# Kernel tuning notes

Hardware: AMD Instinct MI355X
Metric: run time of the kernel (lower is better)

The kernel has to match this reference:

```python
import jax, jax.numpy as jnp
import numpy as np

N_NODES = 50000
N_EDGES = 1250000
VOCAB = 50000
EMBED = 64
HIDDEN = 64
NUM_REL = 3
N_CLASSES = 2
N_GRAPHS = 512


def setup_inputs() -> dict:
    key = jax.random.key(0)
    ks = jax.random.split(key, 12)
    x = jax.random.randint(ks[0], (N_NODES,), 0, VOCAB, dtype=jnp.int32)
    edge_index = jax.random.randint(ks[1], (2, N_EDGES), 0, N_NODES, dtype=jnp.int32)
    edge_type = jax.random.randint(ks[2], (N_EDGES,), 0, NUM_REL, dtype=jnp.int32)
    batch = jnp.sort(jax.random.randint(ks[3], (N_NODES,), 0, N_GRAPHS, dtype=jnp.int32))
    s = 0.05
    emb = jax.random.normal(ks[4], (VOCAB, EMBED), jnp.float32) * s
    w1_rel = jax.random.normal(ks[5], (NUM_REL, EMBED, HIDDEN), jnp.float32) * s
    w1_root = jax.random.normal(ks[6], (EMBED, HIDDEN), jnp.float32) * s
    b1 = jnp.zeros((HIDDEN,), jnp.float32)
    w2_rel = jax.random.normal(ks[7], (NUM_REL, HIDDEN, HIDDEN), jnp.float32) * s
    w2_root = jax.random.normal(ks[8], (HIDDEN, HIDDEN), jnp.float32) * s
    b2 = jnp.zeros((HIDDEN,), jnp.float32)
    lin_w = jax.random.normal(ks[9], (HIDDEN, N_CLASSES), jnp.float32) * s
    lin_b = jnp.zeros((N_CLASSES,), jnp.float32)
    return {"x": x, "edge_index": edge_index, "edge_type": edge_type, "batch": batch,
            "emb": emb, "w1_rel": w1_rel, "w1_root": w1_root, "b1": b1,
            "w2_rel": w2_rel, "w2_root": w2_root, "b2": b2,
            "lin_w": lin_w, "lin_b": lin_b}


def rgcn_conv(h, src, dst, edge_type, w_rel, w_root, bias):
    # PyG RGCNConv: out = h @ W_root + bias + sum_r mean-aggregated (h_src @ W_r)
    out = h @ w_root + bias
    h_src = h[src]  # [E, F] gather
    for r in range(NUM_REL):
        mask = (edge_type == r).astype(h.dtype)  # [E]
        m = (h_src @ w_rel[r]) * mask[:, None]   # [E, H]
        s = jax.ops.segment_sum(m, dst, num_segments=N_NODES)
        cnt = jax.ops.segment_sum(mask, dst, num_segments=N_NODES)
        out = out + s / jnp.maximum(cnt, 1.0)[:, None]
    return out


def reference(x, edge_index, edge_type, batch, emb, w1_rel, w1_root, b1,
              w2_rel, w2_root, b2, lin_w, lin_b):
    src, dst = edge_index[0], edge_index[1]
    emb_eff = emb.at[0].set(0.0)  # padding_idx=0
    h = emb_eff[x]  # [N, EMBED]
    h = jax.nn.relu(rgcn_conv(h, src, dst, edge_type, w1_rel, w1_root, b1))
    h = jax.nn.relu(rgcn_conv(h, src, dst, edge_type, w2_rel, w2_root, b2))
    # global mean pool over graphs
    sums = jax.ops.segment_sum(h, batch, num_segments=N_GRAPHS)
    cnt = jax.ops.segment_sum(jnp.ones((h.shape[0],), h.dtype), batch, num_segments=N_GRAPHS)
    pooled = sums / jnp.maximum(cnt, 1.0)[:, None]  # [G, HIDDEN]
    return pooled @ lin_w + lin_b  # [G, N_CLASSES]
```

## Files before the change

### kernel.cpp

```cpp
#include <hip/hip_runtime.h>

#define CHUNK 2048

__global__ __launch_bounds__(256) void embed_count_kernel(
    const int* __restrict__ x, const float* __restrict__ emb, float* __restrict__ h0,
    const int* __restrict__ ei, int* __restrict__ pcount,
    int n_nodes, int n_edges, int n_bkt, int n_chk, int embed_blocks)
{
    __shared__ int cnt[512];
    int t = threadIdx.x;
    if ((int)blockIdx.x < embed_blocks) {
        int tt = blockIdx.x * 256 + t;
        if (tt < n_nodes * 16) {
            int n = tt >> 4, q = tt & 15;
            int xv = x[n];
            float4 v = {0.f, 0.f, 0.f, 0.f};
            if (xv != 0) v = *(const float4*)(emb + (size_t)xv * 64 + q * 4);
            *(float4*)(h0 + (size_t)n * 64 + q * 4) = v;
        }
        return;
    }
    int jb = blockIdx.x - embed_blocks;
    for (int b = t; b < 512; b += 256) cnt[b] = 0;
    __syncthreads();
    int base = jb * CHUNK;
#pragma unroll
    for (int i = 0; i < CHUNK / 256; ++i) {
        int e = base + i * 256 + t;
        if (e < n_edges) atomicAdd(&cnt[ei[n_edges + e] >> 7], 1);
    }
    __syncthreads();
    for (int b = t; b < n_bkt; b += 256) pcount[b * n_chk + jb] = cnt[b];
}

__global__ __launch_bounds__(256) void colscan_kernel(
    const int* __restrict__ pcount, int* __restrict__ pre,
    int* __restrict__ totals, int* __restrict__ rowstartR,
    const int* __restrict__ batch, const float* __restrict__ linb,
    float* __restrict__ inv_cnt, float* __restrict__ outg,
    int n_chk, int n_bkt, int n_edges, int n_nodes, int n_graphs)
{
    __shared__ int ps[256];
    int b = blockIdx.x, t = threadIdx.x;
    if (b >= n_bkt) {
        int g = (b - n_bkt) * 256 + t;
        if (g < n_graphs) {
            int lo = 0, hi = n_nodes;
            while (lo < hi) { int mid = (lo + hi) >> 1; if (batch[mid] < g) lo = mid + 1; else hi = mid; }
            int s = lo;
            lo = 0; hi = n_nodes;
            while (lo < hi) { int mid = (lo + hi) >> 1; if (batch[mid] < g + 1) lo = mid + 1; else hi = mid; }
            inv_cnt[g] = 1.f / (float)max(lo - s, 1);
            outg[2 * g + 0] = linb[0];
            outg[2 * g + 1] = linb[1];
        }
        return;
    }
    if (b == 0 && t == 0) rowstartR[4 * n_nodes] = n_edges;
    int v[4], s = 0;
#pragma unroll
    for (int i = 0; i < 4; ++i) {
        int jj = t * 4 + i;
        v[i] = (jj < n_chk) ? pcount[b * n_chk + jj] : 0;
        s += v[i];
    }
    ps[t] = s;
    __syncthreads();
    for (int o = 1; o < 256; o <<= 1) {
        int u = (t >= o) ? ps[t - o] : 0;
        __syncthreads();
        ps[t] += u;
        __syncthreads();
    }
    int run = (t > 0) ? ps[t - 1] : 0;
#pragma unroll
    for (int i = 0; i < 4; ++i) {
        int jj = t * 4 + i;
        if (jj < n_chk) pre[jj * n_bkt + b] = run;
        run += v[i];
    }
    if (t == 255) totals[b] = run;
}

__global__ __launch_bounds__(256) void scatter_kernel(
    const int* __restrict__ ei, const int* __restrict__ et,
    const int* __restrict__ pre, const int* __restrict__ totals,
    int* __restrict__ esort, int* __restrict__ bucket_start,
    int n_edges, int n_bkt)
{
    __shared__ int bs[512], fill2[512], ps[256];
    int t = threadIdx.x, j = blockIdx.x;
    int a0 = (2 * t < n_bkt) ? totals[2 * t] : 0;
    int a1 = (2 * t + 1 < n_bkt) ? totals[2 * t + 1] : 0;
    ps[t] = a0 + a1;
    __syncthreads();
    for (int o = 1; o < 256; o <<= 1) {
        int u = (t >= o) ? ps[t - o] : 0;
        __syncthreads();
        ps[t] += u;
        __syncthreads();
    }
    int basex = (t > 0) ? ps[t - 1] : 0;
    bs[2 * t] = basex;
    bs[2 * t + 1] = basex + a0;
    fill2[t] = 0; fill2[t + 256] = 0;
    __syncthreads();
    if (j == 0) {
        for (int b = t; b < n_bkt; b += 256) bucket_start[b] = bs[b];
        if (t == 0) bucket_start[n_bkt] = n_edges;
    }
    for (int b = t; b < n_bkt; b += 256) bs[b] += pre[j * n_bkt + b];
    __syncthreads();
    int base = j * CHUNK;
#pragma unroll
    for (int i = 0; i < CHUNK / 256; ++i) {
        int e = base + i * 256 + t;
        if (e < n_edges) {
            int s = ei[e], d = ei[n_edges + e], r = et[e];
            int b = d >> 7;
            int pos = bs[b] + atomicAdd(&fill2[b], 1);
            esort[pos] = s | (r << 16) | ((d & 127) << 18);
        }
    }
}

__global__ __launch_bounds__(256) void bucket_sort_kernel(
    const int* __restrict__ bucket_start, const int* __restrict__ esort_in,
    int* __restrict__ esort_out, int* __restrict__ rowstartR, int n_nodes)
{
    __shared__ int cnt[512], off[512], fill[512], ps[256];
    int t = threadIdx.x, b = blockIdx.x;
    int s = bucket_start[b], e = bucket_start[b + 1];
    cnt[t] = 0; cnt[t + 256] = 0; fill[t] = 0; fill[t + 256] = 0;
    __syncthreads();
    for (int i = s + t; i < e; i += 256)
        atomicAdd(&cnt[(esort_in[i] >> 16) & 0x1FF], 1);
    __syncthreads();
    int a0 = cnt[2 * t], a1 = cnt[2 * t + 1];
    ps[t] = a0 + a1;
    __syncthreads();
    for (int o = 1; o < 256; o <<= 1) {
        int v = (t >= o) ? ps[t - o] : 0;
        __syncthreads();
        ps[t] += v;
        __syncthreads();
    }
    int basex = (t > 0) ? ps[t - 1] : 0;
    off[2 * t] = basex;
    off[2 * t + 1] = basex + a0;
    __syncthreads();
    int d0 = b * 128 + (2 * t >> 2);
    if (d0 < n_nodes) rowstartR[b * 512 + 2 * t] = s + off[2 * t];
    int d1 = b * 128 + ((2 * t + 1) >> 2);
    if (d1 < n_nodes) rowstartR[b * 512 + 2 * t + 1] = s + off[2 * t + 1];
    __syncthreads();
    for (int i = s + t; i < e; i += 256) {
        int p = esort_in[i];
        int bin = (p >> 16) & 0x1FF;
        int pos = s + off[bin] + atomicAdd(&fill[bin], 1);
        esort_out[pos] = p;
    }
}

__global__ __launch_bounds__(256) void agg_kernel(
    const float* __restrict__ hin, const int* __restrict__ rowstartR,
    const int* __restrict__ esort, float* __restrict__ means, int n_nodes)
{
    int wid = (blockIdx.x * 256 + threadIdx.x) >> 6;
    int lane = threadIdx.x & 63;
    if (wid >= n_nodes) return;
    int q = lane >> 4;
    int c = lane & 15;
    int4 rs = *(const int4*)(rowstartR + wid * 4);
    int s = rs.x, e = rs.w;

    float4 a0 = {0.f,0.f,0.f,0.f}, a1 = {0.f,0.f,0.f,0.f}, a2 = {0.f,0.f,0.f,0.f};

    int i = s + 4 * q;
    for (; i + 4 <= e; i += 16) {
        int p0 = esort[i], p1 = esort[i + 1], p2 = esort[i + 2], p3 = esort[i + 3];
        float4 v0 = *(const float4*)(hin + (size_t)(p0 & 0xFFFF) * 64 + c * 4);
        float4 v1 = *(const float4*)(hin + (size_t)(p1 & 0xFFFF) * 64 + c * 4);
        float4 v2 = *(const float4*)(hin + (size_t)(p2 & 0xFFFF) * 64 + c * 4);
        float4 v3 = *(const float4*)(hin + (size_t)(p3 & 0xFFFF) * 64 + c * 4);
#pragma unroll
        for (int m = 0; m < 4; ++m) {
            int p = m == 0 ? p0 : m == 1 ? p1 : m == 2 ? p2 : p3;
            float4 v = m == 0 ? v0 : m == 1 ? v1 : m == 2 ? v2 : v3;
            int r = (p >> 16) & 3;
            float m0 = (r == 0) ? 1.f : 0.f;
            float m1 = (r == 1) ? 1.f : 0.f;
            float m2 = (r == 2) ? 1.f : 0.f;
            a0.x = fmaf(m0, v.x, a0.x); a0.y = fmaf(m0, v.y, a0.y);
            a0.z = fmaf(m0, v.z, a0.z); a0.w = fmaf(m0, v.w, a0.w);
            a1.x = fmaf(m1, v.x, a1.x); a1.y = fmaf(m1, v.y, a1.y);
            a1.z = fmaf(m1, v.z, a1.z); a1.w = fmaf(m1, v.w, a1.w);
            a2.x = fmaf(m2, v.x, a2.x); a2.y = fmaf(m2, v.y, a2.y);
            a2.z = fmaf(m2, v.z, a2.z); a2.w = fmaf(m2, v.w, a2.w);
        }
    }
#pragma unroll
    for (int m = 0; m < 3; ++m) {
        int ii = i + m;
        if (ii < e) {
            int p = esort[ii];
            float4 v = *(const float4*)(hin + (size_t)(p & 0xFFFF) * 64 + c * 4);
            int r = (p >> 16) & 3;
            float m0 = (r == 0) ? 1.f : 0.f;
            float m1 = (r == 1) ? 1.f : 0.f;
            float m2 = (r == 2) ? 1.f : 0.f;
            a0.x = fmaf(m0, v.x, a0.x); a0.y = fmaf(m0, v.y, a0.y);
            a0.z = fmaf(m0, v.z, a0.z); a0.w = fmaf(m0, v.w, a0.w);
            a1.x = fmaf(m1, v.x, a1.x); a1.y = fmaf(m1, v.y, a1.y);
            a1.z = fmaf(m1, v.z, a1.z); a1.w = fmaf(m1, v.w, a1.w);
            a2.x = fmaf(m2, v.x, a2.x); a2.y = fmaf(m2, v.y, a2.y);
            a2.z = fmaf(m2, v.z, a2.z); a2.w = fmaf(m2, v.w, a2.w);
        }
    }
#pragma unroll
    for (int off = 16; off < 64; off <<= 1) {
        a0.x += __shfl_xor(a0.x, off); a0.y += __shfl_xor(a0.y, off);
        a0.z += __shfl_xor(a0.z, off); a0.w += __shfl_xor(a0.w, off);
        a1.x += __shfl_xor(a1.x, off); a1.y += __shfl_xor(a1.y, off);
        a1.z += __shfl_xor(a1.z, off); a1.w += __shfl_xor(a1.w, off);
        a2.x += __shfl_xor(a2.x, off); a2.y += __shfl_xor(a2.y, off);
        a2.z += __shfl_xor(a2.z, off); a2.w += __shfl_xor(a2.w, off);
    }
    if (q < 3) {
        int cnt = (q == 0) ? (rs.y - rs.x) : (q == 1) ? (rs.z - rs.y) : (rs.w - rs.z);
        float4 a = (q == 0) ? a0 : (q == 1) ? a1 : a2;
        float inv = 1.f / (float)max(cnt, 1);
        float4 m = {a.x * inv, a.y * inv, a.z * inv, a.w * inv};
        *(float4*)(means + (size_t)wid * 192 + q * 64 + c * 4) = m;
    }
}

__device__ __forceinline__ void stage16(const float* gsrc, float* ldst)
{
    __builtin_amdgcn_global_load_lds(
        (const __attribute__((address_space(1))) unsigned int*)gsrc,
        (__attribute__((address_space(3))) unsigned int*)ldst,
        16, 0, 0);
}

__global__ __launch_bounds__(128, 4) void transform_kernel(
    const float* __restrict__ hin, const float* __restrict__ means,
    const float* __restrict__ wroot, const float* __restrict__ wrel,
    const float* __restrict__ bias, float* __restrict__ hout,
    const int* __restrict__ batch, const float* __restrict__ linw,
    const float* __restrict__ inv_cnt, float* __restrict__ outg,
    int n_nodes, int do_pool)
{
    __shared__ float wsh[2][2048];
    __shared__ float gacc[64][2];
    int t = threadIdx.x;
    int gt = blockIdx.x * 128 + t;
    int g = gt >> 4, q = gt & 15;
    int n0 = g * 4;
    bool active = (n0 < n_nodes);

#pragma unroll
    for (int i = 0; i < 4; ++i)
        stage16(wroot + i * 512 + t * 4, wsh[0] + i * 512 + t * 4);

    float4 acc[4];
    {
        float4 b = {0.f, 0.f, 0.f, 0.f};
        if (active) b = *(const float4*)(bias + q * 4);
#pragma unroll
        for (int i = 0; i < 4; ++i) acc[i] = b;
    }

    const float* hv = hin + (size_t)n0 * 64;
    const float* mv = means + (size_t)n0 * 192;

    for (int ss = 0; ss < 8; ++ss) {
        __syncthreads();
        if (ss < 7) {
            const float* wsrc = (ss + 1 < 2) ? (wroot + (size_t)(ss + 1) * 2048)
                                             : (wrel + (size_t)(ss - 1) * 2048);
            float* d = wsh[(ss + 1) & 1];
#pragma unroll
            for (int i = 0; i < 4; ++i)
                stage16(wsrc + i * 512 + t * 4, d + i * 512 + t * 4);
        }
        int p  = ss >> 1;
        int kb = (ss & 1) * 32;
        const float* vb = ((p == 0) ? hv : (mv + (p - 1) * 64)) + kb;
        int vst = (p == 0) ? 64 : 192;
        const float* wbuf = wsh[ss & 1];
        if (active) {
#pragma unroll
            for (int k4 = 0; k4 < 8; ++k4) {
                float4 v[4];
#pragma unroll
                for (int i = 0; i < 4; ++i)
                    v[i] = *(const float4*)(vb + i * vst + k4 * 4);
#pragma unroll
                for (int kk = 0; kk < 4; ++kk) {
                    float4 w = *(const float4*)(wbuf + (k4 * 4 + kk) * 64 + q * 4);
#pragma unroll
                    for (int i = 0; i < 4; ++i) {
                        float sv = kk == 0 ? v[i].x : kk == 1 ? v[i].y : kk == 2 ? v[i].z : v[i].w;
                        acc[i].x = fmaf(sv, w.x, acc[i].x);
                        acc[i].y = fmaf(sv, w.y, acc[i].y);
                        acc[i].z = fmaf(sv, w.z, acc[i].z);
                        acc[i].w = fmaf(sv, w.w, acc[i].w);
                    }
                }
            }
        }
    }
    if (!do_pool) {
        if (active) {
            float* o = hout + (size_t)n0 * 64 + q * 4;
#pragma unroll
            for (int i = 0; i < 4; ++i) {
                float4 r = {fmaxf(acc[i].x, 0.f), fmaxf(acc[i].y, 0.f),
                            fmaxf(acc[i].z, 0.f), fmaxf(acc[i].w, 0.f)};
                *(float4*)(o + i * 64) = r;
            }
        }
    } else {
        if (t < 64) { gacc[t][0] = 0.f; gacc[t][1] = 0.f; }
        __syncthreads();
        int nbase = blockIdx.x * 32;
        int gmin = batch[min(nbase, n_nodes - 1)];
        if (active) {
            float4 lwA = *(const float4*)(linw + q * 8);
            float4 lwB = *(const float4*)(linw + q * 8 + 4);
            float d0[4], d1[4];
#pragma unroll
            for (int i = 0; i < 4; ++i) {
                float4 r = {fmaxf(acc[i].x, 0.f), fmaxf(acc[i].y, 0.f),
                            fmaxf(acc[i].z, 0.f), fmaxf(acc[i].w, 0.f)};
                d0[i] = r.x * lwA.x + r.y * lwA.z + r.z * lwB.x + r.w * lwB.z;
                d1[i] = r.x * lwA.y + r.y * lwA.w + r.z * lwB.y + r.w * lwB.w;
            }
#pragma unroll
            for (int off = 1; off < 16; off <<= 1) {
#pragma unroll
                for (int i = 0; i < 4; ++i) {
                    d0[i] += __shfl_xor(d0[i], off);
                    d1[i] += __shfl_xor(d1[i], off);
                }
            }
            if (q == 0) {
#pragma unroll
                for (int i = 0; i < 4; ++i) {
                    int n = n0 + i;
                    if (n < n_nodes) {
                        int gg = batch[n];
                        float ic = inv_cnt[gg];
                        int idx = gg - gmin;
                        if (idx < 64) {
                            atomicAdd(&gacc[idx][0], d0[i] * ic);
                            atomicAdd(&gacc[idx][1], d1[i] * ic);
                        } else {
                            atomicAdd(&outg[2 * gg + 0], d0[i] * ic);
                            atomicAdd(&outg[2 * gg + 1], d1[i] * ic);
                        }
                    }
                }
            }
        }
        __syncthreads();
        if (t < 64) {
            float v0 = gacc[t][0], v1 = gacc[t][1];
            if (v0 != 0.f || v1 != 0.f) {
                atomicAdd(&outg[2 * (gmin + t) + 0], v0);
                atomicAdd(&outg[2 * (gmin + t) + 1], v1);
            }
        }
    }
}

extern "C" void kernel_launch(void* const* d_in, const int* in_sizes, int n_in,
                              void* d_out, int out_size, void* d_ws, size_t ws_size,
                              hipStream_t stream)
{
    const int*   x      = (const int*)d_in[0];
    const int*   ei     = (const int*)d_in[1];
    const int*   et     = (const int*)d_in[2];
    const int*   batch  = (const int*)d_in[3];
    const float* emb    = (const float*)d_in[4];
    const float* w1rel  = (const float*)d_in[5];
    const float* w1root = (const float*)d_in[6];
    const float* b1     = (const float*)d_in[7];
    const float* w2rel  = (const float*)d_in[8];
    const float* w2root = (const float*)d_in[9];
    const float* b2     = (const float*)d_in[10];
    const float* linw   = (const float*)d_in[11];
    const float* linb   = (const float*)d_in[12];
    float* out = (float*)d_out;

    const int N = in_sizes[0];
    const int E = in_sizes[2];
    const int G = out_size / 2;
    const int NBKT = (N + 127) >> 7;
    const int NCHK = (E + CHUNK - 1) / CHUNK;

    float* hA        = (float*)d_ws;
    float* hB        = hA + (size_t)N * 64;
    float* means     = hB + (size_t)N * 64;
    int*   esort     = (int*)(means + (size_t)N * 192);
    int*   rowstartR = esort + E;
    int*   bucket_start = rowstartR + 4 * N + 4;
    int*   totals    = bucket_start + NBKT + 1;
    float* inv_cnt   = (float*)(totals + NBKT);
    int*   esort2    = (int*)(inv_cnt + G);
    int*   pcount    = (int*)means + 4 * 1024 * 1024;
    int*   pre       = (int*)means + 5 * 1024 * 1024;

    int embedBlocks = (N * 16 + 255) / 256;
    embed_count_kernel<<<embedBlocks + NCHK, 256, 0, stream>>>(
        x, emb, hA, ei, pcount, N, E, NBKT, NCHK, embedBlocks);
    int gBlocks = (G + 255) / 256;
    colscan_kernel<<<NBKT + gBlocks, 256, 0, stream>>>(
        pcount, pre, totals, rowstartR, batch, linb, inv_cnt, out,
        NCHK, NBKT, E, N, G);
    scatter_kernel<<<NCHK, 256, 0, stream>>>(ei, et, pre, totals, esort, bucket_start, E, NBKT);
    bucket_sort_kernel<<<NBKT, 256, 0, stream>>>(bucket_start, esort, esort2, rowstartR, N);

    int aggBlocks = (N * 64 + 255) / 256;
    int tfBlocks  = (N + 31) / 32;
    agg_kernel<<<aggBlocks, 256, 0, stream>>>(hA, rowstartR, esort2, means, N);
    transform_kernel<<<tfBlocks, 128, 0, stream>>>(
        hA, means, w1root, w1rel, b1, hB, batch, linw, inv_cnt, out, N, 0);
    agg_kernel<<<aggBlocks, 256, 0, stream>>>(hB, rowstartR, esort2, means, N);
    transform_kernel<<<tfBlocks, 128, 0, stream>>>(
        hB, means, w2root, w2rel, b2, hA, batch, linw, inv_cnt, out, N, 1);
}
```

Before: 308.2 us.

## Restructure transform kernel to stage node features in LDS and read weights uniformly

The transform kernel now handles 64 nodes per 256-thread block. Each lane owns one node and each wave owns 16 output columns. Node features and means are staged through a padded, double-buffered LDS tile, and weights are read with wave-uniform addresses, which lets them become scalar loads, instead of being staged through LDS with global_load_lds. This is meant to cut per-thread global vector loads and LDS weight traffic. In exchange it adds more block barriers, more registers for the 16-wide accumulator, and an LDS round trip for the output transpose.

New measurement: 295.1 us. 1.04x faster.

```diff
diff --git a/kernel.cpp b/kernel.cpp
--- a/kernel.cpp
+++ b/kernel.cpp
@@ -235,15 +235,7 @@
     }
 }
 
-__device__ __forceinline__ void stage16(const float* gsrc, float* ldst)
-{
-    __builtin_amdgcn_global_load_lds(
-        (const __attribute__((address_space(1))) unsigned int*)gsrc,
-        (__attribute__((address_space(3))) unsigned int*)ldst,
-        16, 0, 0);
-}
-
-__global__ __launch_bounds__(128, 4) void transform_kernel(
+__global__ __launch_bounds__(256, 4) void transform_kernel(
     const float* __restrict__ hin, const float* __restrict__ means,
     const float* __restrict__ wroot, const float* __restrict__ wrel,
     const float* __restrict__ bias, float* __restrict__ hout,
@@ -251,122 +243,127 @@
     const float* __restrict__ inv_cnt, float* __restrict__ outg,
     int n_nodes, int do_pool)
 {
-    __shared__ float wsh[2][2048];
-    __shared__ float gacc[64][2];
+    __shared__ float smem[2][64 * 68];
     int t = threadIdx.x;
-    int gt = blockIdx.x * 128 + t;
-    int g = gt >> 4, q = gt & 15;
-    int n0 = g * 4;
-    bool active = (n0 < n_nodes);
-
-#pragma unroll
-    for (int i = 0; i < 4; ++i)
-        stage16(wroot + i * 512 + t * 4, wsh[0] + i * 512 + t * 4);
-
-    float4 acc[4];
-    {
-        float4 b = {0.f, 0.f, 0.f, 0.f};
-        if (active) b = *(const float4*)(bias + q * 4);
-#pragma unroll
-        for (int i = 0; i < 4; ++i) acc[i] = b;
-    }
-
-    const float* hv = hin + (size_t)n0 * 64;
-    const float* mv = means + (size_t)n0 * 192;
-
-    for (int ss = 0; ss < 8; ++ss) {
-        __syncthreads();
-        if (ss < 7) {
-            const float* wsrc = (ss + 1 < 2) ? (wroot + (size_t)(ss + 1) * 2048)
-                                             : (wrel + (size_t)(ss - 1) * 2048);
-            float* d = wsh[(ss + 1) & 1];
-#pragma unroll
-            for (int i = 0; i < 4; ++i)
-                stage16(wsrc + i * 512 + t * 4, d + i * 512 + t * 4);
-        }
-        int p  = ss >> 1;
-        int kb = (ss & 1) * 32;
-        const float* vb = ((p == 0) ? hv : (mv + (p - 1) * 64)) + kb;
-        int vst = (p == 0) ? 64 : 192;
-        const float* wbuf = wsh[ss & 1];
-        if (active) {
-#pragma unroll
-            for (int k4 = 0; k4 < 8; ++k4) {
-                float4 v[4];
-#pragma unroll
-                for (int i = 0; i < 4; ++i)
-                    v[i] = *(const float4*)(vb + i * vst + k4 * 4);
-#pragma unroll
-                for (int kk = 0; kk < 4; ++kk) {
-                    float4 w = *(const float4*)(wbuf + (k4 * 4 + kk) * 64 + q * 4);
-#pragma unroll
-                    for (int i = 0; i < 4; ++i) {
-                        float sv = kk == 0 ? v[i].x : kk == 1 ? v[i].y : kk == 2 ? v[i].z : v[i].w;
-                        acc[i].x = fmaf(sv, w.x, acc[i].x);
-                        acc[i].y = fmaf(sv, w.y, acc[i].y);
-                        acc[i].z = fmaf(sv, w.z, acc[i].z);
-                        acc[i].w = fmaf(sv, w.w, acc[i].w);
-                    }
+    int lane = t & 63;
+    int wv = __builtin_amdgcn_readfirstlane(t >> 6);
+    int j0 = wv * 16;
+    int n0g = blockIdx.x * 64;
+
+    int sn_ = t >> 4;
+    int sk  = (t & 15) * 4;
+
+    float4 stg[4];
+#pragma unroll
+    for (int r = 0; r < 4; ++r) {
+        int node = r * 16 + sn_;
+        int gn = min(n0g + node, n_nodes - 1);
+        stg[r] = *(const float4*)(hin + (size_t)gn * 64 + sk);
+    }
+#pragma unroll
+    for (int r = 0; r < 4; ++r) {
+        int node = r * 16 + sn_;
+        *(float4*)&smem[0][node * 68 + sk] = stg[r];
+    }
+
+    float acc[16];
+#pragma unroll
+    for (int i = 0; i < 16; ++i) acc[i] = bias[j0 + i];
+    __syncthreads();
+
+    for (int p = 0; p < 4; ++p) {
+        if (p < 3) {
+#pragma unroll
+            for (int r = 0; r < 4; ++r) {
+                int node = r * 16 + sn_;
+                int gn = min(n0g + node, n_nodes - 1);
+                stg[r] = *(const float4*)(means + (size_t)gn * 192 + p * 64 + sk);
+            }
+        }
+        const float* wb = ((p == 0) ? wroot : (wrel + (size_t)(p - 1) * 4096)) + j0;
+        const float* lv = &smem[p & 1][lane * 68];
+#pragma unroll 4
+        for (int k4 = 0; k4 < 16; ++k4) {
+            float4 v = *(const float4*)(lv + k4 * 4);
+#pragma unroll
+            for (int kk = 0; kk < 4; ++kk) {
+                float vk = kk == 0 ? v.x : kk == 1 ? v.y : kk == 2 ? v.z : v.w;
+                const float* wr = wb + (k4 * 4 + kk) * 64;
+#pragma unroll
+                for (int i = 0; i < 16; ++i)
+                    acc[i] = fmaf(vk, wr[i], acc[i]);
+            }
+        }
+        if (p < 3) {
+            __syncthreads();
+#pragma unroll
+            for (int r = 0; r < 4; ++r) {
+                int node = r * 16 + sn_;
+                *(float4*)&smem[(p + 1) & 1][node * 68 + sk] = stg[r];
+            }
+            __syncthreads();
+        }
+    }
+
+    if (!do_pool) {
+        __syncthreads();
+        float* osh = smem[0];
+#pragma unroll
+        for (int i4 = 0; i4 < 4; ++i4) {
+            float4 r;
+            r.x = fmaxf(acc[i4 * 4 + 0], 0.f);
+            r.y = fmaxf(acc[i4 * 4 + 1], 0.f);
+            r.z = fmaxf(acc[i4 * 4 + 2], 0.f);
+            r.w = fmaxf(acc[i4 * 4 + 3], 0.f);
+            *(float4*)&osh[lane * 68 + j0 + i4 * 4] = r;
+        }
+        __syncthreads();
+#pragma unroll
+        for (int r = 0; r < 4; ++r) {
+            int node = r * 16 + sn_;
+            int gn = n0g + node;
+            if (gn < n_nodes)
+                *(float4*)(hout + (size_t)gn * 64 + sk) =
+                    *(const float4*)&osh[node * 68 + sk];
+        }
+    } else {
+        float d0 = 0.f, d1 = 0.f;
+#pragma unroll
+        for (int i = 0; i < 16; ++i) {
+            float rr = fmaxf(acc[i], 0.f);
+            d0 = fmaf(rr, linw[(j0 + i) * 2 + 0], d0);
+            d1 = fmaf(rr, linw[(j0 + i) * 2 + 1], d1);
+        }
+        __syncthreads();
+        float* wsum = smem[0];
+        float* gacc = smem[0] + 512;
+        wsum[(wv * 64 + lane) * 2 + 0] = d0;
+        wsum[(wv * 64 + lane) * 2 + 1] = d1;
+        if (t < 128) gacc[t] = 0.f;
+        __syncthreads();
+        int gmin = batch[min(n0g, n_nodes - 1)];
+        if (t < 64) {
+            int gn = n0g + t;
+            if (gn < n_nodes) {
+                float s0 = wsum[t * 2]     + wsum[128 + t * 2] +
+                           wsum[256 + t * 2] + wsum[384 + t * 2];
+                float s1 = wsum[t * 2 + 1]     + wsum[128 + t * 2 + 1] +
+                           wsum[256 + t * 2 + 1] + wsum[384 + t * 2 + 1];
+                int gg = batch[gn];
+                float ic = inv_cnt[gg];
+                int idx = gg - gmin;
+                if (idx < 64) {
+                    atomicAdd(&gacc[idx * 2 + 0], s0 * ic);
+                    atomicAdd(&gacc[idx * 2 + 1], s1 * ic);
+                } else {
+                    atomicAdd(&outg[2 * gg + 0], s0 * ic);
+                    atomicAdd(&outg[2 * gg + 1], s1 * ic);
                 }
             }
         }
-    }
-    if (!do_pool) {
-        if (active) {
-            float* o = hout + (size_t)n0 * 64 + q * 4;
-#pragma unroll
-            for (int i = 0; i < 4; ++i) {
-                float4 r = {fmaxf(acc[i].x, 0.f), fmaxf(acc[i].y, 0.f),
-                            fmaxf(acc[i].z, 0.f), fmaxf(acc[i].w, 0.f)};
-                *(float4*)(o + i * 64) = r;
-            }
-        }
-    } else {
-        if (t < 64) { gacc[t][0] = 0.f; gacc[t][1] = 0.f; }
-        __syncthreads();
-        int nbase = blockIdx.x * 32;
-        int gmin = batch[min(nbase, n_nodes - 1)];
-        if (active) {
-            float4 lwA = *(const float4*)(linw + q * 8);
-            float4 lwB = *(const float4*)(linw + q * 8 + 4);
-            float d0[4], d1[4];
-#pragma unroll
-            for (int i = 0; i < 4; ++i) {
-                float4 r = {fmaxf(acc[i].x, 0.f), fmaxf(acc[i].y, 0.f),
-                            fmaxf(acc[i].z, 0.f), fmaxf(acc[i].w, 0.f)};
-                d0[i] = r.x * lwA.x + r.y * lwA.z + r.z * lwB.x + r.w * lwB.z;
-                d1[i] = r.x * lwA.y + r.y * lwA.w + r.z * lwB.y + r.w * lwB.w;
-            }
-#pragma unroll
-            for (int off = 1; off < 16; off <<= 1) {
-#pragma unroll
-                for (int i = 0; i < 4; ++i) {
-                    d0[i] += __shfl_xor(d0[i], off);
-                    d1[i] += __shfl_xor(d1[i], off);
-                }
-            }
-            if (q == 0) {
-#pragma unroll
-                for (int i = 0; i < 4; ++i) {
-                    int n = n0 + i;
-                    if (n < n_nodes) {
-                        int gg = batch[n];
-                        float ic = inv_cnt[gg];
-                        int idx = gg - gmin;
-                        if (idx < 64) {
-                            atomicAdd(&gacc[idx][0], d0[i] * ic);
-                            atomicAdd(&gacc[idx][1], d1[i] * ic);
-                        } else {
-                            atomicAdd(&outg[2 * gg + 0], d0[i] * ic);
-                            atomicAdd(&outg[2 * gg + 1], d1[i] * ic);
-                        }
-                    }
-                }
-            }
-        }
         __syncthreads();
         if (t < 64) {
-            float v0 = gacc[t][0], v1 = gacc[t][1];
+            float v0 = gacc[t * 2], v1 = gacc[t * 2 + 1];
             if (v0 != 0.f || v1 != 0.f) {
                 atomicAdd(&outg[2 * (gmin + t) + 0], v0);
                 atomicAdd(&outg[2 * (gmin + t) + 1], v1);
@@ -423,11 +420,11 @@
     bucket_sort_kernel<<<NBKT, 256, 0, stream>>>(bucket_start, esort, esort2, rowstartR, N);
 
     int aggBlocks = (N * 64 + 255) / 256;
-    int tfBlocks  = (N + 31) / 32;
+    int tfBlocks  = (N + 63) / 64;
     agg_kernel<<<aggBlocks, 256, 0, stream>>>(hA, rowstartR, esort2, means, N);
-    transform_kernel<<<tfBlocks, 128, 0, stream>>>(
+    transform_kernel<<<tfBlocks, 256, 0, stream>>>(
         hA, means, w1root, w1rel, b1, hB, batch, linw, inv_cnt, out, N, 0);
     agg_kernel<<<aggBlocks, 256, 0, stream>>>(hB, rowstartR, esort2, means, N);
-    transform_kernel<<<tfBlocks, 128, 0, stream>>>(
+    transform_kernel<<<tfBlocks, 256, 0, stream>>>(
         hB, means, w2root, w2rel, b2, hA, batch, linw, inv_cnt, out, N, 1);
 }
```
